# Performance work log

Measured on AMD Instinct MI355X. Metric: run time of the kernel, lower is better.

Reference implementation:

```python
import jax, jax.numpy as jnp
import numpy as np

B, D, V = 64, 4096, 50257
SAMPLE_KEY = 42  # fixed key for the multinomial draw


def setup_inputs() -> dict:
    key = jax.random.key(0)
    k1, k2, k3, k4 = jax.random.split(key, 4)
    hidden_states = jax.random.normal(k1, (B, D), jnp.float32)
    embd_weight = jax.random.normal(k2, (V, D), jnp.float32) * 0.02
    # temperature in [0.5, 1.5) to avoid div-by-near-zero; top_p in [0.1, 1.0)
    temperature = 0.5 + jax.random.uniform(k3, (B,), jnp.float32)
    top_p = 0.1 + 0.9 * jax.random.uniform(k4, (B,), jnp.float32)
    return {
        "hidden_states": hidden_states,
        "embd_weight": embd_weight,
        "temperature": temperature,
        "top_p": top_p,
    }


def reference(hidden_states, embd_weight, temperature, top_p):
    # logits = h @ W^T / temperature  -> [B, V]
    logits = jnp.matmul(hidden_states, embd_weight.T) / temperature[:, None]
    # descending sort (torch sort(descending=True))
    idx = jnp.argsort(-logits, axis=-1)                      # [B, V] int
    sorted_logits = jnp.take_along_axis(logits, idx, axis=-1)
    sorted_probs = jax.nn.softmax(sorted_logits, axis=-1)
    cum = jnp.cumsum(sorted_probs, axis=-1)
    # exclusive cumsum > top_p  => mask out tail of the nucleus
    mask = (cum - sorted_probs) > top_p[:, None]
    sorted_logits = jnp.where(mask, -jnp.inf, sorted_logits)
    # unsort back to vocab order: argsort of the permutation is its inverse
    inv = jnp.argsort(idx, axis=-1)
    masked_logits = jnp.take_along_axis(sorted_logits, inv, axis=-1)
    # torch: probs = softmax(logits); multinomial(probs, 1)
    # jax.random.categorical on logits samples the identical distribution.
    ids = jax.random.categorical(jax.random.key(SAMPLE_KEY), masked_logits, axis=-1)
    return ids
```

## Files before the change

kernel.cpp:

```cpp
#include <hip/hip_runtime.h>
#include <stdint.h>

#ifndef GUMBEL_SCHEME
#define GUMBEL_SCHEME 1
#endif

constexpr int B_ = 64;
constexpr int D_ = 4096;
constexpr int V_ = 50257;

__device__ __forceinline__ void tf_round(uint32_t& x0, uint32_t& x1, int r) {
  x0 += x1;
  x1 = (x1 << r) | (x1 >> (32 - r));
  x1 ^= x0;
}

__device__ __forceinline__ void threefry2x32(uint32_t xx0, uint32_t xx1,
                                             uint32_t& y0, uint32_t& y1) {
  const uint32_t k0 = 0u, k1 = 42u;
  const uint32_t k2 = 0x1BD11BDAu ^ k0 ^ k1;
  uint32_t x0 = xx0 + k0, x1 = xx1 + k1;
  tf_round(x0, x1, 13); tf_round(x0, x1, 15); tf_round(x0, x1, 26); tf_round(x0, x1, 6);
  x0 += k1; x1 += k2 + 1u;
  tf_round(x0, x1, 17); tf_round(x0, x1, 29); tf_round(x0, x1, 16); tf_round(x0, x1, 24);
  x0 += k2; x1 += k0 + 2u;
  tf_round(x0, x1, 13); tf_round(x0, x1, 15); tf_round(x0, x1, 26); tf_round(x0, x1, 6);
  x0 += k0; x1 += k1 + 3u;
  tf_round(x0, x1, 17); tf_round(x0, x1, 29); tf_round(x0, x1, 16); tf_round(x0, x1, 24);
  x0 += k1; x1 += k2 + 4u;
  tf_round(x0, x1, 13); tf_round(x0, x1, 15); tf_round(x0, x1, 26); tf_round(x0, x1, 6);
  x0 += k2; x1 += k0 + 5u;
  y0 = x0; y1 = x1;
}

__device__ __forceinline__ uint32_t rand_bits(uint32_t flat_idx) {
  uint32_t y0, y1;
#if GUMBEL_SCHEME
  threefry2x32(0u, flat_idx, y0, y1);
  return y0 ^ y1;
#else
  const uint32_t HALF = (uint32_t)(B_ * (long)V_ / 2);
  uint32_t j = (flat_idx < HALF) ? flat_idx : flat_idx - HALF;
  threefry2x32(j, j + HALF, y0, y1);
  return (flat_idx < HALF) ? y0 : y1;
#endif
}

__device__ __forceinline__ float gumbel_from_bits(uint32_t r) {
  float f = __uint_as_float((r >> 9) | 0x3F800000u) - 1.0f;
  float u = fmaxf(1.17549435e-38f, f);
  return -logf(-logf(u));
}

__device__ __forceinline__ uint32_t f2mono(float f) {
  uint32_t u = __float_as_uint(f);
  return u ^ (0x80000000u | (uint32_t)((int32_t)u >> 31));
}
__device__ __forceinline__ float mono2f(uint32_t m) {
  uint32_t u = (m & 0x80000000u) ? (m ^ 0x80000000u) : ~m;
  return __uint_as_float(u);
}

__global__ __launch_bounds__(256) void gemm_logits(
    const float* __restrict__ H, const float* __restrict__ W,
    const float* __restrict__ T, float* __restrict__ logits) {
  constexpr int TN = 128, BK = 64;
  __shared__ float Ash[64][BK + 4];
  __shared__ float Bsh[BK][TN + 4];

  const int tid = threadIdx.x;
  const int tx = tid & 15;
  const int ty = tid >> 4;
  const int n0 = blockIdx.x * TN;

  float acc[4][8];
#pragma unroll
  for (int i = 0; i < 4; i++)
#pragma unroll
    for (int j = 0; j < 8; j++) acc[i][j] = 0.f;

  for (int k0 = 0; k0 < D_; k0 += BK) {
#pragma unroll
    for (int i = 0; i < 4; i++) {
      const int li = tid + i * 256;
      const int row = li >> 4, c4 = li & 15;
      const float4 v = *(const float4*)(H + (size_t)row * D_ + k0 + (c4 << 2));
      *(float4*)&Ash[row][c4 << 2] = v;
    }
#pragma unroll
    for (int i = 0; i < 8; i++) {
      const int li = tid + i * 256;
      const int row = li >> 4, c4 = li & 15;
      int gr = n0 + row; gr = (gr < V_) ? gr : (V_ - 1);
      const float4 v = *(const float4*)(W + (size_t)gr * D_ + k0 + (c4 << 2));
      Bsh[(c4 << 2) + 0][row] = v.x;
      Bsh[(c4 << 2) + 1][row] = v.y;
      Bsh[(c4 << 2) + 2][row] = v.z;
      Bsh[(c4 << 2) + 3][row] = v.w;
    }
    __syncthreads();
#pragma unroll
    for (int kk = 0; kk < BK; kk += 4) {
      float4 a[4], b0[4], b1[4];
#pragma unroll
      for (int i2 = 0; i2 < 4; i2++) a[i2] = *(const float4*)&Ash[(ty << 2) + i2][kk];
#pragma unroll
      for (int t = 0; t < 4; t++) {
        b0[t] = *(const float4*)&Bsh[kk + t][tx << 2];
        b1[t] = *(const float4*)&Bsh[kk + t][64 + (tx << 2)];
      }
#pragma unroll
      for (int i2 = 0; i2 < 4; i2++) {
#pragma unroll
        for (int t = 0; t < 4; t++) {
          const float av = ((const float*)&a[i2])[t];
          const float* bp0 = (const float*)&b0[t];
          const float* bp1 = (const float*)&b1[t];
#pragma unroll
          for (int j = 0; j < 4; j++) {
            acc[i2][j]     = fmaf(av, bp0[j], acc[i2][j]);
            acc[i2][j + 4] = fmaf(av, bp1[j], acc[i2][j + 4]);
          }
        }
      }
    }
    __syncthreads();
  }

#pragma unroll
  for (int i2 = 0; i2 < 4; i2++) {
    const int mrow = (ty << 2) + i2;
    const float tmp = T[mrow];
#pragma unroll
    for (int j = 0; j < 8; j++) {
      const int n = n0 + ((j < 4) ? ((tx << 2) + j) : (64 + (tx << 2) + (j - 4)));
      if (n < V_) logits[(size_t)mrow * V_ + n] = acc[i2][j] / tmp;
    }
  }
}

constexpr int TPB = 1024;
constexpr int NPER = (V_ + TPB - 1) / TPB;
static_assert(NPER * TPB >= V_, "coverage");

__device__ float blk_reduce_sum(float v, volatile float* red, float* bc) {
  const int tid = threadIdx.x;
#pragma unroll
  for (int off = 32; off > 0; off >>= 1) v += __shfl_down(v, off);
  if ((tid & 63) == 0) red[tid >> 6] = v;
  __syncthreads();
  if (tid == 0) {
    float s = 0.f;
#pragma unroll
    for (int w = 0; w < 16; w++) s += red[w];
    *bc = s;
  }
  __syncthreads();
  const float r = *bc;
  __syncthreads();
  return r;
}

__device__ float blk_reduce_max(float v, volatile float* red, float* bc) {
  const int tid = threadIdx.x;
#pragma unroll
  for (int off = 32; off > 0; off >>= 1) v = fmaxf(v, __shfl_down(v, off));
  if ((tid & 63) == 0) red[tid >> 6] = v;
  __syncthreads();
  if (tid == 0) {
    float s = -INFINITY;
#pragma unroll
    for (int w = 0; w < 16; w++) s = fmaxf(s, red[w]);
    *bc = s;
  }
  __syncthreads();
  const float r = *bc;
  __syncthreads();
  return r;
}

__global__ __launch_bounds__(TPB) void topp_sample(
    float* __restrict__ logits, const float* __restrict__ top_p,
    int* __restrict__ out) {
  __shared__ float red[16];
  __shared__ float bcf;
  __shared__ float redv[16];
  __shared__ int redi[16];
  __shared__ int wct[16];
  __shared__ int runbase;

  const int b = blockIdx.x;
  const int tid = threadIdx.x;
  float* __restrict__ L = logits + (size_t)b * V_;

  float l[NPER];
#pragma unroll
  for (int i = 0; i < NPER; i++) {
    const int v = tid + i * TPB;
    l[i] = (v < V_) ? L[v] : -INFINITY;
  }

  float m = -INFINITY;
#pragma unroll
  for (int i = 0; i < NPER; i++) m = fmaxf(m, l[i]);
  const float M = blk_reduce_max(m, red, &bcf);

  float zl = 0.f;
#pragma unroll
  for (int i = 0; i < NPER; i++) zl += expf(l[i] - M);
  const float Z = blk_reduce_sum(zl, red, &bcf);
  const float P = top_p[b] * Z;

  uint32_t lo = 0x007FFFFFu;
  uint32_t hi = f2mono(M);
  float s_hi = 0.f;
  while (hi - lo > 1u) {
    const uint32_t mid = lo + ((hi - lo) >> 1);
    const float c = mono2f(mid);
    float sl = 0.f;
#pragma unroll
    for (int i = 0; i < NPER; i++) sl += (l[i] > c) ? expf(l[i] - M) : 0.f;
    const float s = blk_reduce_sum(sl, red, &bcf);
    if (s <= P) { hi = mid; s_hi = s; } else { lo = mid; }
  }
  const float cstar = mono2f(hi);

  float ntl = 0.f;
#pragma unroll
  for (int i = 0; i < NPER; i++) ntl += (l[i] == cstar) ? 1.f : 0.f;
  const int n_tie = (int)blk_reduce_sum(ntl, red, &bcf);
  const float p_num = expf(cstar - M);
  int kk = 0;
  {
    float s = s_hi;
    for (int j = 0; j < n_tie; j++) {
      if (s <= P) { kk++; s += p_num; } else break;
    }
  }
  if (kk < n_tie) {
    if (tid == 0) runbase = 0;
    __syncthreads();
    for (int i = 0; i < NPER; i++) {
      const int v = tid + i * TPB;
      const bool tie = (v < V_) && (l[i] == cstar);
      const unsigned long long mk = __ballot(tie);
      const int wid = tid >> 6, lane = tid & 63;
      if (lane == 0) wct[wid] = __popcll(mk);
      __syncthreads();
      int pre = runbase;
      for (int w = 0; w < wid; w++) pre += wct[w];
      if (lane) pre += __popcll(mk & ((~0ull) >> (64 - lane)));
      if (tie && pre >= kk) L[v] = -INFINITY;
      __syncthreads();
      if (tid == 0) {
        int t = 0;
        for (int w = 0; w < 16; w++) t += wct[w];
        runbase += t;
      }
      __syncthreads();
    }
  }

  float best = -INFINITY;
  int bidx = 0x7FFFFFFF;
  for (int i = 0; i < NPER; i++) {
    const int v = tid + i * TPB;
    if (v >= V_) break;
    const float lv = L[v];
    const uint32_t gi = (uint32_t)(b * V_ + v);
    const float g = gumbel_from_bits(rand_bits(gi));
    const float val = (lv >= cstar) ? (g + lv) : -INFINITY;
    if (val > best) { best = val; bidx = v; }
  }
#pragma unroll
  for (int off = 32; off > 0; off >>= 1) {
    const float ov = __shfl_down(best, off);
    const int oi = __shfl_down(bidx, off);
    if (ov > best || (ov == best && oi < bidx)) { best = ov; bidx = oi; }
  }
  const int wid = tid >> 6, lane = tid & 63;
  if (lane == 0) { redv[wid] = best; redi[wid] = bidx; }
  __syncthreads();
  if (tid == 0) {
    float bv = redv[0]; int bi = redi[0];
    for (int w = 1; w < 16; w++)
      if (redv[w] > bv || (redv[w] == bv && redi[w] < bi)) { bv = redv[w]; bi = redi[w]; }
    out[b] = bi;
  }
}

extern "C" void kernel_launch(void* const* d_in, const int* in_sizes, int n_in,
                              void* d_out, int out_size, void* d_ws, size_t ws_size,
                              hipStream_t stream) {
  const float* H = (const float*)d_in[0];
  const float* W = (const float*)d_in[1];
  const float* T = (const float*)d_in[2];
  const float* topp = (const float*)d_in[3];
  float* logits = (float*)d_ws;
  int* out = (int*)d_out;

  const int nblk = (V_ + 127) / 128;
  gemm_logits<<<dim3(nblk), dim3(256), 0, stream>>>(H, W, T, logits);
  topp_sample<<<dim3(B_), dim3(TPB), 0, stream>>>(logits, topp, out);
}
```

Baseline: 1.439 ms.

## Split-K GEMM with atomics, swizzled LDS, and radix-histogram top-p threshold search

The GEMM is split over K in two halves that accumulate into a zeroed workspace with float atomics. The B tile in shared memory gets an XOR swizzle to cut bank conflicts, and the temperature division moves into the sampling kernel. The sampler replaces a ~32-step bisection over the float bit pattern, which needs one block reduction per step, with a three-level radix histogram using fixed-point 64-bit shared-memory atomics. Tie masking now stays in registers instead of writing back to global memory. Costs: an extra zeroing kernel, atomic contention, nondeterministic summation order, and fixed-point quantisation that could shift the threshold slightly.

```diff
diff --git a/kernel.cpp b/kernel.cpp
--- a/kernel.cpp
+++ b/kernel.cpp
@@ -61,9 +61,12 @@
   return __uint_as_float(u);
 }
 
-__global__ __launch_bounds__(256) void gemm_logits(
+constexpr int SPLITK = 2;
+constexpr int KSEG = D_ / SPLITK;
+
+__global__ __launch_bounds__(256, 3) void gemm_logits(
     const float* __restrict__ H, const float* __restrict__ W,
-    const float* __restrict__ T, float* __restrict__ logits) {
+    float* __restrict__ logits) {
   constexpr int TN = 128, BK = 64;
   __shared__ float Ash[64][BK + 4];
   __shared__ float Bsh[BK][TN + 4];
@@ -72,6 +75,7 @@
   const int tx = tid & 15;
   const int ty = tid >> 4;
   const int n0 = blockIdx.x * TN;
+  const int kbeg = blockIdx.y * KSEG;
 
   float acc[4][8];
 #pragma unroll
@@ -79,7 +83,7 @@
 #pragma unroll
     for (int j = 0; j < 8; j++) acc[i][j] = 0.f;
 
-  for (int k0 = 0; k0 < D_; k0 += BK) {
+  for (int k0 = kbeg; k0 < kbeg + KSEG; k0 += BK) {
 #pragma unroll
     for (int i = 0; i < 4; i++) {
       const int li = tid + i * 256;
@@ -93,21 +97,24 @@
       const int row = li >> 4, c4 = li & 15;
       int gr = n0 + row; gr = (gr < V_) ? gr : (V_ - 1);
       const float4 v = *(const float4*)(W + (size_t)gr * D_ + k0 + (c4 << 2));
-      Bsh[(c4 << 2) + 0][row] = v.x;
-      Bsh[(c4 << 2) + 1][row] = v.y;
-      Bsh[(c4 << 2) + 2][row] = v.z;
-      Bsh[(c4 << 2) + 3][row] = v.w;
+      const int sw = ((((row >> 2) ^ (c4 & 7)) << 2) | (row & 3));
+      Bsh[(c4 << 2) + 0][sw] = v.x;
+      Bsh[(c4 << 2) + 1][sw] = v.y;
+      Bsh[(c4 << 2) + 2][sw] = v.z;
+      Bsh[(c4 << 2) + 3][sw] = v.w;
     }
     __syncthreads();
 #pragma unroll
     for (int kk = 0; kk < BK; kk += 4) {
+      const int cxor = (kk >> 2) & 7;
+      const int qb = (tx ^ cxor) << 2;
       float4 a[4], b0[4], b1[4];
 #pragma unroll
       for (int i2 = 0; i2 < 4; i2++) a[i2] = *(const float4*)&Ash[(ty << 2) + i2][kk];
 #pragma unroll
       for (int t = 0; t < 4; t++) {
-        b0[t] = *(const float4*)&Bsh[kk + t][tx << 2];
-        b1[t] = *(const float4*)&Bsh[kk + t][64 + (tx << 2)];
+        b0[t] = *(const float4*)&Bsh[kk + t][qb];
+        b1[t] = *(const float4*)&Bsh[kk + t][64 + qb];
       }
 #pragma unroll
       for (int i2 = 0; i2 < 4; i2++) {
@@ -130,18 +137,24 @@
 #pragma unroll
   for (int i2 = 0; i2 < 4; i2++) {
     const int mrow = (ty << 2) + i2;
-    const float tmp = T[mrow];
 #pragma unroll
     for (int j = 0; j < 8; j++) {
       const int n = n0 + ((j < 4) ? ((tx << 2) + j) : (64 + (tx << 2) + (j - 4)));
-      if (n < V_) logits[(size_t)mrow * V_ + n] = acc[i2][j] / tmp;
-    }
-  }
+      if (n < V_) atomicAdd(&logits[(size_t)mrow * V_ + n], acc[i2][j]);
+    }
+  }
+}
+
+__global__ __launch_bounds__(256) void zero_ws(float4* __restrict__ p, int n4) {
+  int i = blockIdx.x * blockDim.x + threadIdx.x;
+  const int stride = gridDim.x * blockDim.x;
+  for (; i < n4; i += stride) p[i] = make_float4(0.f, 0.f, 0.f, 0.f);
 }
 
 constexpr int TPB = 1024;
 constexpr int NPER = (V_ + TPB - 1) / TPB;
 static_assert(NPER * TPB >= V_, "coverage");
+constexpr int NB1 = 4096;
 
 __device__ float blk_reduce_sum(float v, volatile float* red, float* bc) {
   const int tid = threadIdx.x;
@@ -179,11 +192,68 @@
   return r;
 }
 
+__device__ void level_select(unsigned long long* hist, int NB,
+                             unsigned long long P_in, double frac, int tid,
+                             unsigned long long* wsum, int* selb_p,
+                             unsigned long long* selA_p,
+                             int& b_out, unsigned long long& A_out,
+                             unsigned long long& Tot_out,
+                             unsigned long long& P_out) {
+  const int lane = tid & 63, wid = tid >> 6;
+  const int nchunk = NB >> 2;
+  const int nwav = nchunk >> 6;
+  unsigned long long c = 0ull;
+  if (tid < nchunk)
+    c = hist[4 * tid] + hist[4 * tid + 1] + hist[4 * tid + 2] + hist[4 * tid + 3];
+  unsigned long long x = c;
+#pragma unroll
+  for (int off = 1; off < 64; off <<= 1) {
+    unsigned long long y = __shfl_up(x, (unsigned int)off);
+    if (lane >= off) x += y;
+  }
+  if (tid < nchunk && lane == 63) wsum[wid] = x;
+  if (tid == 0) *selb_p = 0x7FFFFFFF;
+  __syncthreads();
+  unsigned long long woff = 0ull, Tot = 0ull;
+  for (int w = 0; w < nwav; w++) {
+    const unsigned long long ws = wsum[w];
+    if (w < wid) woff += ws;
+    Tot += ws;
+  }
+  const unsigned long long P =
+      (frac >= 0.0) ? (unsigned long long)(frac * (double)Tot) : P_in;
+  if (tid < nchunk) {
+    unsigned long long cs = woff + (x - c);
+    for (int j = 0; j < 4; j++) {
+      const unsigned long long hv = hist[4 * tid + j];
+      cs += hv;
+      if (hv > 0ull && (Tot - cs) <= P) atomicMin(selb_p, 4 * tid + j);
+    }
+  }
+  __syncthreads();
+  const int sb = *selb_p;
+  if (tid == (sb >> 2)) {
+    unsigned long long cs = woff + (x - c);
+    for (int j = 0; j <= (sb & 3); j++) cs += hist[4 * tid + j];
+    *selA_p = Tot - cs;
+  }
+  __syncthreads();
+  b_out = sb;
+  A_out = *selA_p;
+  Tot_out = Tot;
+  P_out = P;
+  __syncthreads();
+}
+
 __global__ __launch_bounds__(TPB) void topp_sample(
-    float* __restrict__ logits, const float* __restrict__ top_p,
-    int* __restrict__ out) {
+    const float* __restrict__ logits, const float* __restrict__ T,
+    const float* __restrict__ top_p, int* __restrict__ out) {
   __shared__ float red[16];
   __shared__ float bcf;
+  __shared__ unsigned long long hist[NB1];
+  __shared__ unsigned long long wsum[16];
+  __shared__ int selb;
+  __shared__ unsigned long long selA;
   __shared__ float redv[16];
   __shared__ int redi[16];
   __shared__ int wct[16];
@@ -191,44 +261,91 @@
 
   const int b = blockIdx.x;
   const int tid = threadIdx.x;
-  float* __restrict__ L = logits + (size_t)b * V_;
+  const int lane = tid & 63, wid = tid >> 6;
+  const float tb = T[b];
+  const float* __restrict__ L = logits + (size_t)b * V_;
 
   float l[NPER];
 #pragma unroll
   for (int i = 0; i < NPER; i++) {
     const int v = tid + i * TPB;
-    l[i] = (v < V_) ? L[v] : -INFINITY;
-  }
-
-  float m = -INFINITY;
-#pragma unroll
-  for (int i = 0; i < NPER; i++) m = fmaxf(m, l[i]);
-  const float M = blk_reduce_max(m, red, &bcf);
-
-  float zl = 0.f;
-#pragma unroll
-  for (int i = 0; i < NPER; i++) zl += expf(l[i] - M);
+    l[i] = (v < V_) ? (L[v] / tb) : -INFINITY;
+  }
+
+  float m0 = -INFINITY;
+#pragma unroll
+  for (int i = 0; i < NPER; i++) m0 = fmaxf(m0, l[i]);
+  const float M = blk_reduce_max(m0, red, &bcf);
+
+  int b1, b2, b3;
+  unsigned long long A1, A2, A3, Tot1, TotD, P1, P2, P3, PD;
+
+  for (int k = tid; k < NB1; k += TPB) hist[k] = 0ull;
+  __syncthreads();
+#pragma unroll
+  for (int i = 0; i < NPER; i++) {
+    const int v = tid + i * TPB;
+    if (v < V_) {
+      const uint32_t mm = f2mono(l[i]);
+      const float e = expf(l[i] - M);
+      atomicAdd(&hist[mm >> 20], (unsigned long long)(e * 4294967296.0f));
+    }
+  }
+  __syncthreads();
+  level_select(hist, NB1, 0ull, (double)top_p[b], tid, wsum, &selb, &selA,
+               b1, A1, Tot1, P1);
+
+  for (int k = tid; k < NB1; k += TPB) hist[k] = 0ull;
+  __syncthreads();
+#pragma unroll
+  for (int i = 0; i < NPER; i++) {
+    const int v = tid + i * TPB;
+    if (v < V_) {
+      const uint32_t mm = f2mono(l[i]);
+      if ((int)(mm >> 20) == b1) {
+        const float e = expf(l[i] - M);
+        atomicAdd(&hist[(mm >> 8) & 0xFFFu], (unsigned long long)(e * 4294967296.0f));
+      }
+    }
+  }
+  __syncthreads();
+  P2 = P1 - A1;
+  level_select(hist, NB1, P2, -1.0, tid, wsum, &selb, &selA, b2, A2, TotD, PD);
+
+  for (int k = tid; k < 256; k += TPB) hist[k] = 0ull;
+  __syncthreads();
+  const uint32_t hi24 = ((uint32_t)b1 << 12) | (uint32_t)b2;
+#pragma unroll
+  for (int i = 0; i < NPER; i++) {
+    const int v = tid + i * TPB;
+    if (v < V_) {
+      const uint32_t mm = f2mono(l[i]);
+      if ((mm >> 8) == hi24) {
+        const float e = expf(l[i] - M);
+        atomicAdd(&hist[mm & 0xFFu], (unsigned long long)(e * 4294967296.0f));
+      }
+    }
+  }
+  __syncthreads();
+  P3 = P2 - A2;
+  level_select(hist, 256, P3, -1.0, tid, wsum, &selb, &selA, b3, A3, TotD, PD);
+
+  const uint32_t cmono = ((uint32_t)b1 << 20) | ((uint32_t)b2 << 8) | (uint32_t)b3;
+  const float cstar = mono2f(cmono);
+
+  float zl = 0.f, sl = 0.f, ntl = 0.f;
+#pragma unroll
+  for (int i = 0; i < NPER; i++) {
+    const float e = expf(l[i] - M);
+    zl += e;
+    sl += (l[i] > cstar) ? e : 0.f;
+    ntl += (l[i] == cstar) ? 1.f : 0.f;
+  }
   const float Z = blk_reduce_sum(zl, red, &bcf);
+  const float s_hi = blk_reduce_sum(sl, red, &bcf);
+  const int n_tie = (int)blk_reduce_sum(ntl, red, &bcf);
   const float P = top_p[b] * Z;
 
-  uint32_t lo = 0x007FFFFFu;
-  uint32_t hi = f2mono(M);
-  float s_hi = 0.f;
-  while (hi - lo > 1u) {
-    const uint32_t mid = lo + ((hi - lo) >> 1);
-    const float c = mono2f(mid);
-    float sl = 0.f;
-#pragma unroll
-    for (int i = 0; i < NPER; i++) sl += (l[i] > c) ? expf(l[i] - M) : 0.f;
-    const float s = blk_reduce_sum(sl, red, &bcf);
-    if (s <= P) { hi = mid; s_hi = s; } else { lo = mid; }
-  }
-  const float cstar = mono2f(hi);
-
-  float ntl = 0.f;
-#pragma unroll
-  for (int i = 0; i < NPER; i++) ntl += (l[i] == cstar) ? 1.f : 0.f;
-  const int n_tie = (int)blk_reduce_sum(ntl, red, &bcf);
   const float p_num = expf(cstar - M);
   int kk = 0;
   {
@@ -240,17 +357,17 @@
   if (kk < n_tie) {
     if (tid == 0) runbase = 0;
     __syncthreads();
+#pragma unroll
     for (int i = 0; i < NPER; i++) {
       const int v = tid + i * TPB;
       const bool tie = (v < V_) && (l[i] == cstar);
       const unsigned long long mk = __ballot(tie);
-      const int wid = tid >> 6, lane = tid & 63;
       if (lane == 0) wct[wid] = __popcll(mk);
       __syncthreads();
       int pre = runbase;
       for (int w = 0; w < wid; w++) pre += wct[w];
       if (lane) pre += __popcll(mk & ((~0ull) >> (64 - lane)));
-      if (tie && pre >= kk) L[v] = -INFINITY;
+      if (tie && pre >= kk) l[i] = -INFINITY;
       __syncthreads();
       if (tid == 0) {
         int t = 0;
@@ -263,14 +380,16 @@
 
   float best = -INFINITY;
   int bidx = 0x7FFFFFFF;
+#pragma unroll
   for (int i = 0; i < NPER; i++) {
     const int v = tid + i * TPB;
-    if (v >= V_) break;
-    const float lv = L[v];
-    const uint32_t gi = (uint32_t)(b * V_ + v);
-    const float g = gumbel_from_bits(rand_bits(gi));
-    const float val = (lv >= cstar) ? (g + lv) : -INFINITY;
-    if (val > best) { best = val; bidx = v; }
+    if (v < V_) {
+      const float lv = l[i];
+      const uint32_t gi = (uint32_t)(b * V_ + v);
+      const float g = gumbel_from_bits(rand_bits(gi));
+      const float val = (lv >= cstar) ? (g + lv) : -INFINITY;
+      if (val > best) { best = val; bidx = v; }
+    }
   }
 #pragma unroll
   for (int off = 32; off > 0; off >>= 1) {
@@ -278,7 +397,6 @@
     const int oi = __shfl_down(bidx, off);
     if (ov > best || (ov == best && oi < bidx)) { best = ov; bidx = oi; }
   }
-  const int wid = tid >> 6, lane = tid & 63;
   if (lane == 0) { redv[wid] = best; redi[wid] = bidx; }
   __syncthreads();
   if (tid == 0) {
@@ -299,7 +417,10 @@
   float* logits = (float*)d_ws;
   int* out = (int*)d_out;
 
+  const int n4 = (B_ * V_) / 4;
+  zero_ws<<<dim3(2048), dim3(256), 0, stream>>>((float4*)logits, n4);
+
   const int nblk = (V_ + 127) / 128;
-  gemm_logits<<<dim3(nblk), dim3(256), 0, stream>>>(H, W, T, logits);
-  topp_sample<<<dim3(B_), dim3(TPB), 0, stream>>>(logits, topp, out);
-}
+  gemm_logits<<<dim3(nblk, SPLITK), dim3(256), 0, stream>>>(H, W, logits);
+  topp_sample<<<dim3(B_), dim3(TPB), 0, stream>>>(logits, T, topp, out);
+}
```

Measured after the change: 1.412 ms. Within noise of the previous version (-1.9%).
